# Kernel tuning notes

Hardware: AMD Instinct MI355X
Metric: run time of the kernel (lower is better)

The kernel has to match this reference:

```python
import jax, jax.numpy as jnp
import numpy as np
import math

D_IN = 4096
D_OUT = 4096
RANK = 8
SCALE = 16.0 / 8.0  # alpha / rank


def fwht(x):
    """Fast Walsh-Hadamard transform over last dim (power of two), orthonormal."""
    d = x.shape[-1]
    orig_shape = x.shape
    h = 1
    while h < d:
        y = x.reshape(x.shape[:-1] + (d // (2 * h), 2, h))
        a = y[..., 0, :]
        b = y[..., 1, :]
        x = jnp.stack([a + b, a - b], axis=-2).reshape(orig_shape)
        h <<= 1
    return x / math.sqrt(d)


def srht_right_multiply(x, signs, perm):
    # x @ P  (sign flip -> column permutation -> FWHT)
    return fwht((x * signs)[..., perm])


def srht_right_multiply_T(x, signs, inv_perm):
    # x @ P^T (FWHT -> inverse permutation -> sign flip)
    return fwht(x)[..., inv_perm] * signs


def setup_inputs() -> dict:
    key = jax.random.key(0)
    ks = jax.random.split(key, 10)
    x = jax.random.normal(ks[0], (4, 2048, D_IN), dtype=jnp.float32)
    W = jax.random.normal(ks[1], (D_OUT, D_IN), dtype=jnp.float32) * 0.02
    b = jax.random.normal(ks[2], (D_OUT,), dtype=jnp.float32) * 0.02
    # kaiming-uniform-ish init for A; random B (real module zero-inits B, but
    # random B exercises the full adapter path for correctness checking)
    bound = 1.0 / math.sqrt(D_IN)
    A = jax.random.uniform(ks[3], (RANK, D_IN), minval=-bound, maxval=bound, dtype=jnp.float32)
    B = jax.random.normal(ks[4], (D_OUT, RANK), dtype=jnp.float32) * 0.02
    in_signs = (jax.random.randint(ks[5], (D_IN,), 0, 2) * 2 - 1).astype(jnp.float32)
    out_signs = (jax.random.randint(ks[6], (D_OUT,), 0, 2) * 2 - 1).astype(jnp.float32)
    in_perm = jax.random.permutation(ks[7], D_IN).astype(jnp.int32)
    in_inv_perm = jnp.argsort(in_perm).astype(jnp.int32)
    out_perm = jax.random.permutation(ks[8], D_OUT).astype(jnp.int32)
    out_inv_perm = jnp.argsort(out_perm).astype(jnp.int32)
    return {
        "x": x, "W": W, "b": b, "A": A, "B": B,
        "in_signs": in_signs, "out_signs": out_signs,
        "in_perm": in_perm, "in_inv_perm": in_inv_perm,
        "out_perm": out_perm, "out_inv_perm": out_inv_perm,
    }


def reference(x, W, b, A, B, in_signs, out_signs, in_perm, in_inv_perm, out_perm, out_inv_perm):
    # base linear
    residual = jnp.einsum('bsi,oi->bso', x, W) + b
    # adapter path: x @ P_in^T @ A^T @ B^T @ P_out, scaled
    adapter_in = srht_right_multiply_T(x, in_signs, in_inv_perm)  # [b,s,in]
    down = jnp.einsum('bsi,ri->bsr', adapter_in, A)               # [b,s,rank]
    up = jnp.einsum('bsr,or->bso', down, B)                       # [b,s,out]
    up = srht_right_multiply(up, out_signs, out_perm)
    return residual + SCALE * up
```

## Files before the change

### kernel.cpp

```cpp
#include <hip/hip_runtime.h>
#include <stdint.h>
#include <stddef.h>

#define DDIM 4096
#define MROWS 8192
#define RANK 8

typedef __attribute__((ext_vector_type(8))) short bf16x8;
typedef __attribute__((ext_vector_type(4))) float f32x4;
typedef __attribute__((ext_vector_type(16))) float f32x16;
typedef __attribute__((ext_vector_type(4))) unsigned short u16x4;
typedef __attribute__((ext_vector_type(8))) unsigned short u16x8;

__device__ __forceinline__ unsigned short f2bf(float f) {
  union { float f; unsigned int u; } c; c.f = f;
  unsigned int u = c.u + 0x7fffu + ((c.u >> 16) & 1u);
  return (unsigned short)(u >> 16);
}

__global__ void convert_x_kernel(const float4* __restrict__ x, u16x8* __restrict__ out) {
  int idx = blockIdx.x * 256 + threadIdx.x;
  float4 v0 = x[2 * idx];
  float4 v1 = x[2 * idx + 1];
  u16x8 o;
  o[0] = f2bf(v0.x); o[1] = f2bf(v0.y); o[2] = f2bf(v0.z); o[3] = f2bf(v0.w);
  o[4] = f2bf(v1.x); o[5] = f2bf(v1.y); o[6] = f2bf(v1.z); o[7] = f2bf(v1.w);
  out[idx] = o;
}

__global__ __launch_bounds__(1024) void srht_fold_kernel(
    const float* __restrict__ A, const float* __restrict__ Bm,
    const float* __restrict__ in_signs, const float* __restrict__ out_signs,
    const int* __restrict__ in_perm, const int* __restrict__ out_perm,
    float* __restrict__ A2, float* __restrict__ B2t) {
  __shared__ float buf[DDIM];
  const int tid = threadIdx.x;
  const int b = blockIdx.x;
  if (b < RANK) {
    const int r = b;
    for (int j = tid; j < DDIM; j += 1024) {
      int p = in_perm[j];
      buf[j] = in_signs[p] * A[r * DDIM + p];
    }
  } else {
    const int r = b - RANK;
    for (int j = tid; j < DDIM; j += 1024) {
      int p = out_perm[j];
      buf[j] = out_signs[p] * Bm[p * RANK + r];
    }
  }
  __syncthreads();
  for (int h = 1; h < DDIM; h <<= 1) {
    for (int p = tid; p < DDIM / 2; p += 1024) {
      int j = p & (h - 1);
      int i0 = ((p - j) << 1) + j;
      int i1 = i0 + h;
      float a = buf[i0], c = buf[i1];
      buf[i0] = a + c;
      buf[i1] = a - c;
    }
    __syncthreads();
  }
  const float scale = (b < RANK) ? (1.0f / 64.0f) : (2.0f / 64.0f);
  float* dst = (b < RANK) ? (A2 + b * DDIM) : (B2t + (b - RANK) * DDIM);
  for (int j = tid; j < DDIM; j += 1024) dst[j] = buf[j] * scale;
}

__global__ void weff_kernel(const float4* __restrict__ W, const float* __restrict__ A2,
                            const float* __restrict__ B2t, u16x8* __restrict__ Weff) {
  int idx = blockIdx.x * 256 + threadIdx.x;
  int o = idx >> 9;
  int c8 = idx & 511;
  float4 w0 = W[2 * idx];
  float4 w1 = W[2 * idx + 1];
#pragma unroll
  for (int r = 0; r < RANK; ++r) {
    float s = B2t[r * DDIM + o];
    const float4* av = (const float4*)(A2 + r * DDIM) + 2 * c8;
    float4 a0 = av[0], a1 = av[1];
    w0.x += s * a0.x; w0.y += s * a0.y; w0.z += s * a0.z; w0.w += s * a0.w;
    w1.x += s * a1.x; w1.y += s * a1.y; w1.z += s * a1.z; w1.w += s * a1.w;
  }
  u16x8 u;
  u[0] = f2bf(w0.x); u[1] = f2bf(w0.y); u[2] = f2bf(w0.z); u[3] = f2bf(w0.w);
  u[4] = f2bf(w1.x); u[5] = f2bf(w1.y); u[6] = f2bf(w1.z); u[7] = f2bf(w1.w);
  Weff[idx] = u;
}

__device__ __forceinline__ void async_copy16(const unsigned short* g, unsigned short* l) {
  __builtin_amdgcn_global_load_lds(
      (const __attribute__((address_space(1))) unsigned int*)g,
      (__attribute__((address_space(3))) unsigned int*)l, 16, 0, 0);
}

__global__ __launch_bounds__(256) void gemm_bt_kernel(
    const unsigned short* __restrict__ Ab,
    const unsigned short* __restrict__ Bb,
    const float* __restrict__ bias,
    float* __restrict__ C) {
  constexpr int K = 4096, N = 4096;
  __shared__ unsigned short As[128 * 64];
  __shared__ unsigned short Bs[128 * 64];

  const int tid = threadIdx.x;
  const int pid = blockIdx.x;

  const int GRID_N = 32;
  const int grpsz = 8 * GRID_N;
  const int group = pid / grpsz;
  const int lpid = pid % grpsz;
  const int m_blk = group * 8 + (lpid & 7);
  const int n_blk = lpid >> 3;

  const int mBase = m_blk * 128;
  const int nBase = n_blk * 128;

  const int sr = tid >> 3;
  const int swz_s = (sr & 7) ^ ((sr >> 3) & 3);
  const int sc = (tid & 7) ^ swz_s;
  const unsigned short* ga[4];
  const unsigned short* gb[4];
#pragma unroll
  for (int j = 0; j < 4; ++j) {
    ga[j] = Ab + (size_t)(mBase + j * 32 + sr) * K + sc * 8;
    gb[j] = Bb + (size_t)(nBase + j * 32 + sr) * K + sc * 8;
  }
  unsigned short* lA = As + tid * 8;
  unsigned short* lB = Bs + tid * 8;

  const int lane = tid & 63;
  const int wid = tid >> 6;
  const int wm = wid >> 1;
  const int wn = wid & 1;
  const int lm = lane & 31;
  const int half = lane >> 5;
  const int swz_f = (lm & 7) ^ ((lm >> 3) & 3);

  int aoff[2][4], boff[2][4];
#pragma unroll
  for (int mt = 0; mt < 2; ++mt) {
    int r = wm * 64 + mt * 32 + lm;
#pragma unroll
    for (int ks = 0; ks < 4; ++ks) {
      int c = ks * 2 + half;
      aoff[mt][ks] = r * 64 + ((c ^ swz_f) * 8);
    }
  }
#pragma unroll
  for (int nt = 0; nt < 2; ++nt) {
    int r = wn * 64 + nt * 32 + lm;
#pragma unroll
    for (int ks = 0; ks < 4; ++ks) {
      int c = ks * 2 + half;
      boff[nt][ks] = r * 64 + ((c ^ swz_f) * 8);
    }
  }

  f32x16 acc[2][2];
#pragma unroll
  for (int mt = 0; mt < 2; ++mt)
#pragma unroll
    for (int nt = 0; nt < 2; ++nt)
#pragma unroll
      for (int i = 0; i < 16; ++i) acc[mt][nt][i] = 0.f;

  for (int kt = 0; kt < K / 64; ++kt) {
#pragma unroll
    for (int j = 0; j < 4; ++j) async_copy16(ga[j], lA + j * 2048);
#pragma unroll
    for (int j = 0; j < 4; ++j) async_copy16(gb[j], lB + j * 2048);
#pragma unroll
    for (int j = 0; j < 4; ++j) { ga[j] += 64; gb[j] += 64; }
    __syncthreads();
#pragma unroll
    for (int ks = 0; ks < 4; ++ks) {
      bf16x8 af[2], bfr[2];
#pragma unroll
      for (int mt = 0; mt < 2; ++mt) af[mt] = *(const bf16x8*)(As + aoff[mt][ks]);
#pragma unroll
      for (int nt = 0; nt < 2; ++nt) bfr[nt] = *(const bf16x8*)(Bs + boff[nt][ks]);
#pragma unroll
      for (int mt = 0; mt < 2; ++mt)
#pragma unroll
        for (int nt = 0; nt < 2; ++nt)
          acc[mt][nt] = __builtin_amdgcn_mfma_f32_32x32x16_bf16(af[mt], bfr[nt],
                                                                acc[mt][nt], 0, 0, 0);
    }
    __syncthreads();
  }

#pragma unroll
  for (int nt = 0; nt < 2; ++nt) {
    const int col = nBase + wn * 64 + nt * 32 + lm;
    const float bc = bias[col];
#pragma unroll
    for (int mt = 0; mt < 2; ++mt) {
      const int row0 = mBase + wm * 64 + mt * 32 + 4 * half;
      float* cp = C + (size_t)row0 * N + col;
#pragma unroll
      for (int reg = 0; reg < 16; ++reg) {
        int row = (reg & 3) + 8 * (reg >> 2);
        cp[(size_t)row * N] = acc[mt][nt][reg] + bc;
      }
    }
  }
}

extern "C" void kernel_launch(void* const* d_in, const int* in_sizes, int n_in,
                              void* d_out, int out_size, void* d_ws, size_t ws_size,
                              hipStream_t stream) {
  const float* x        = (const float*)d_in[0];
  const float* W        = (const float*)d_in[1];
  const float* b        = (const float*)d_in[2];
  const float* A        = (const float*)d_in[3];
  const float* Bm       = (const float*)d_in[4];
  const float* in_signs = (const float*)d_in[5];
  const float* out_signs= (const float*)d_in[6];
  const int*   in_perm  = (const int*)d_in[7];
  const int*   out_perm = (const int*)d_in[9];
  float* out = (float*)d_out;

  char* ws = (char*)d_ws;
  unsigned short* x_bf = (unsigned short*)ws;
  unsigned short* weff = (unsigned short*)(ws + (size_t)67108864);
  float* A2  = (float*)(ws + (size_t)67108864 + (size_t)33554432);
  float* B2t = A2 + RANK * DDIM;

  convert_x_kernel<<<16384, 256, 0, stream>>>((const float4*)x, (u16x8*)x_bf);
  srht_fold_kernel<<<16, 1024, 0, stream>>>(A, Bm, in_signs, out_signs, in_perm, out_perm,
                                            A2, B2t);
  weff_kernel<<<8192, 256, 0, stream>>>((const float4*)W, A2, B2t, (u16x8*)weff);
  gemm_bt_kernel<<<2048, 256, 0, stream>>>(x_bf, weff, b, out);
}
```

Before: 605.1 us.

## Warp-specialize GEMM with producer waves double-buffering LDS tiles

```diff
diff --git a/kernel.cpp b/kernel.cpp
--- a/kernel.cpp
+++ b/kernel.cpp
@@ -9,7 +9,6 @@
 typedef __attribute__((ext_vector_type(8))) short bf16x8;
 typedef __attribute__((ext_vector_type(4))) float f32x4;
 typedef __attribute__((ext_vector_type(16))) float f32x16;
-typedef __attribute__((ext_vector_type(4))) unsigned short u16x4;
 typedef __attribute__((ext_vector_type(8))) unsigned short u16x8;
 
 __device__ __forceinline__ unsigned short f2bf(float f) {
@@ -93,16 +92,18 @@
       (__attribute__((address_space(3))) unsigned int*)l, 16, 0, 0);
 }
 
-__global__ __launch_bounds__(256) void gemm_bt_kernel(
+__global__ __launch_bounds__(512, 4) void gemm_bt_kernel(
     const unsigned short* __restrict__ Ab,
     const unsigned short* __restrict__ Bb,
     const float* __restrict__ bias,
     float* __restrict__ C) {
   constexpr int K = 4096, N = 4096;
-  __shared__ unsigned short As[128 * 64];
-  __shared__ unsigned short Bs[128 * 64];
+  constexpr int BUF = 128 * 64;
+  __shared__ unsigned short As[2 * BUF];
+  __shared__ unsigned short Bs[2 * BUF];
 
   const int tid = threadIdx.x;
+  const int wid = tid >> 6;
   const int pid = blockIdx.x;
 
   const int GRID_N = 32;
@@ -111,25 +112,51 @@
   const int lpid = pid % grpsz;
   const int m_blk = group * 8 + (lpid & 7);
   const int n_blk = lpid >> 3;
-
   const int mBase = m_blk * 128;
   const int nBase = n_blk * 128;
 
-  const int sr = tid >> 3;
-  const int swz_s = (sr & 7) ^ ((sr >> 3) & 3);
-  const int sc = (tid & 7) ^ swz_s;
-  const unsigned short* ga[4];
-  const unsigned short* gb[4];
-#pragma unroll
-  for (int j = 0; j < 4; ++j) {
-    ga[j] = Ab + (size_t)(mBase + j * 32 + sr) * K + sc * 8;
-    gb[j] = Bb + (size_t)(nBase + j * 32 + sr) * K + sc * 8;
-  }
-  unsigned short* lA = As + tid * 8;
-  unsigned short* lB = Bs + tid * 8;
+  if (wid >= 4) {
+    const int pt = tid & 255;
+    const int sr = pt >> 3;
+    const int swz_s = (sr & 7) ^ ((sr >> 3) & 3);
+    const int sc = (pt & 7) ^ swz_s;
+    const unsigned short* ga[4];
+    const unsigned short* gb[4];
+#pragma unroll
+    for (int j = 0; j < 4; ++j) {
+      ga[j] = Ab + (size_t)(mBase + j * 32 + sr) * K + sc * 8;
+      gb[j] = Bb + (size_t)(nBase + j * 32 + sr) * K + sc * 8;
+    }
+    unsigned short* lA = As + pt * 8;
+    unsigned short* lB = Bs + pt * 8;
+
+#pragma unroll
+    for (int j = 0; j < 4; ++j) async_copy16(ga[j], lA + j * 2048);
+#pragma unroll
+    for (int j = 0; j < 4; ++j) async_copy16(gb[j], lB + j * 2048);
+#pragma unroll
+    for (int j = 0; j < 4; ++j) { ga[j] += 64; gb[j] += 64; }
+    __builtin_amdgcn_s_waitcnt(0x0f70);
+    __syncthreads();
+
+    for (int kt = 0; kt < K / 64 - 1; ++kt) {
+      const int nb = (kt + 1) & 1;
+      unsigned short* dA = lA + nb * BUF;
+      unsigned short* dB = lB + nb * BUF;
+#pragma unroll
+      for (int j = 0; j < 4; ++j) async_copy16(ga[j], dA + j * 2048);
+#pragma unroll
+      for (int j = 0; j < 4; ++j) async_copy16(gb[j], dB + j * 2048);
+#pragma unroll
+      for (int j = 0; j < 4; ++j) { ga[j] += 64; gb[j] += 64; }
+      __builtin_amdgcn_s_waitcnt(0x0f70);
+      __syncthreads();
+    }
+    __syncthreads();
+    return;
+  }
 
   const int lane = tid & 63;
-  const int wid = tid >> 6;
   const int wm = wid >> 1;
   const int wn = wid & 1;
   const int lm = lane & 31;
@@ -164,21 +191,18 @@
 #pragma unroll
       for (int i = 0; i < 16; ++i) acc[mt][nt][i] = 0.f;
 
+  __syncthreads();
+
   for (int kt = 0; kt < K / 64; ++kt) {
-#pragma unroll
-    for (int j = 0; j < 4; ++j) async_copy16(ga[j], lA + j * 2048);
-#pragma unroll
-    for (int j = 0; j < 4; ++j) async_copy16(gb[j], lB + j * 2048);
-#pragma unroll
-    for (int j = 0; j < 4; ++j) { ga[j] += 64; gb[j] += 64; }
-    __syncthreads();
+    const unsigned short* as = As + (kt & 1) * BUF;
+    const unsigned short* bs = Bs + (kt & 1) * BUF;
 #pragma unroll
     for (int ks = 0; ks < 4; ++ks) {
       bf16x8 af[2], bfr[2];
 #pragma unroll
-      for (int mt = 0; mt < 2; ++mt) af[mt] = *(const bf16x8*)(As + aoff[mt][ks]);
-#pragma unroll
-      for (int nt = 0; nt < 2; ++nt) bfr[nt] = *(const bf16x8*)(Bs + boff[nt][ks]);
+      for (int mt = 0; mt < 2; ++mt) af[mt] = *(const bf16x8*)(as + aoff[mt][ks]);
+#pragma unroll
+      for (int nt = 0; nt < 2; ++nt) bfr[nt] = *(const bf16x8*)(bs + boff[nt][ks]);
 #pragma unroll
       for (int mt = 0; mt < 2; ++mt)
 #pragma unroll
@@ -230,5 +254,5 @@
   srht_fold_kernel<<<16, 1024, 0, stream>>>(A, Bm, in_signs, out_signs, in_perm, out_perm,
                                             A2, B2t);
   weff_kernel<<<8192, 256, 0, stream>>>((const float4*)W, A2, B2t, (u16x8*)weff);
-  gemm_bt_kernel<<<2048, 256, 0, stream>>>(x_bf, weff, b, out);
-}
+  gemm_bt_kernel<<<2048, 512, 0, stream>>>(x_bf, weff, b, out);
+}
```

Result: slower. 621.0 us (+2.6%).
